# Kernel optimization log

Measured on AMD Instinct MI355X. Metric: run time of the kernel, lower is better.

Reference implementation:

```python
import jax, jax.numpy as jnp
import numpy as np


def setup_inputs() -> dict:
    key = jax.random.key(0)
    ks = jax.random.split(key, 6)
    B, H, KVH, D = 8, 32, 8, 128
    PAGES_PER_SEQ, PAGE_SIZE, L_MAX = 512, 16, 4096
    total_pages = B * PAGES_PER_SEQ  # 4096
    kv_len = PAGES_PER_SEQ * PAGE_SIZE  # 8192 tokens per sequence
    q = jax.random.normal(ks[0], (B, H, 1, D), dtype=jnp.float32)
    paged_kv_cache = jax.random.normal(ks[1], (total_pages, 2, KVH, PAGE_SIZE, D), dtype=jnp.float32)
    kv_page_indptr = (jnp.arange(B + 1, dtype=jnp.int32) * PAGES_PER_SEQ)
    kv_page_indices = jax.random.permutation(ks[2], total_pages).astype(jnp.int32)
    sparse_ind = jax.random.randint(ks[3], (B, H, L_MAX), 0, kv_len, dtype=jnp.int32)
    sparse_nnz = jax.random.randint(ks[4], (B, H), 1, L_MAX + 1, dtype=jnp.int32)
    return {
        "q": q,
        "paged_kv_cache": paged_kv_cache,
        "kv_page_indptr": kv_page_indptr,
        "kv_page_indices": kv_page_indices,
        "sparse_ind": sparse_ind,
        "sparse_nnz": sparse_nnz,
    }


def reference(q, paged_kv_cache, kv_page_indptr, kv_page_indices, sparse_ind, sparse_nnz):
    # q: [B, H, 1, D]; paged_kv_cache: [P, 2, KVH, PS, D]
    B, H, _, D = q.shape
    KVH, PS = paged_kv_cache.shape[2], paged_kv_cache.shape[3]
    groups = H // KVH
    L = sparse_ind.shape[-1]
    scale = jnp.float32(1.0 / (D ** 0.5))

    # Paged-table lookup: token index -> (logical page, offset) -> physical page id
    page_idx = sparse_ind // PS               # [B, H, L]
    off_in_page = sparse_ind % PS             # [B, H, L]
    page_id = kv_page_indices[kv_page_indptr[:B][:, None, None] + page_idx]  # [B, H, L]

    kv_head = (jnp.arange(H) // groups)[None, :, None]  # GQA head mapping, [1, H, 1]
    K = paged_kv_cache[page_id, 0, kv_head, off_in_page]  # [B, H, L, D]
    V = paged_kv_cache[page_id, 1, kv_head, off_in_page]  # [B, H, L, D]

    qk = jnp.einsum("bhd,bhld->bhl", q[:, :, 0, :], K)
    mask = jnp.arange(L)[None, None, :] < sparse_nnz[:, :, None]
    # Kernel uses additive -1e6 for masked lanes (K loaded as 0 -> qk==0)
    scores = jnp.where(mask, qk * scale, jnp.float32(-1e6))
    p = jax.nn.softmax(scores, axis=-1)       # online-softmax is math-equivalent
    out = jnp.einsum("bhl,bhld->bhd", p, V)
    return out[:, :, None, :]                  # [B, H, 1, D]
```

## Files before the change

### kernel.cpp

```cpp
#include <hip/hip_runtime.h>
#include <math.h>

#define BB   8
#define HH   32
#define KVHH 8
#define DD   128
#define PSZ  16
#define LMAX 4096
#define CHUNK 256
#define NCHUNK (LMAX / CHUNK)

#define PAGE_STRIDE (2 * KVHH * PSZ * DD)
#define KV_OFFSET   (KVHH * PSZ * DD)
#define HEAD_STRIDE (PSZ * DD)

__global__ __launch_bounds__(256) void attn_partial(
    const float* __restrict__ q,
    const float* __restrict__ cache,
    const int*   __restrict__ indptr,
    const int*   __restrict__ pageind,
    const int*   __restrict__ sind,
    const int*   __restrict__ snnz,
    float* __restrict__ ws_m,
    float* __restrict__ ws_l,
    float* __restrict__ ws_acc)
{
    const int blk   = blockIdx.x;
    const int xcd   = blk & 7;
    const int slot  = (blk >> 3) & 63;
    const int super = blk >> 9;
    const int g     = super * 8 + xcd;
    const int b     = g >> 3;
    const int kvh   = g & 7;
    const int h     = (kvh << 2) + (slot >> 4);
    const int chunk = slot & 15;
    const int bh    = b * HH + h;
    const int tid   = threadIdx.x;

    const int nnz  = snnz[bh];
    const int l0   = chunk * CHUNK;
    const int widx = bh * NCHUNK + chunk;

    if (l0 >= nnz) {
        if (tid == 0) { ws_m[widx] = -1e30f; ws_l[widx] = 0.0f; }
        if (tid < DD) ws_acc[widx * DD + tid] = 0.0f;
        return;
    }
    const int nrows = min(nnz - l0, CHUNK);
    const int nr32  = (nrows + 31) & ~31;

    __shared__ unsigned s_base[CHUNK];
    __shared__ float    s_p[CHUNK];
    __shared__ float    s_red[16];
    __shared__ float    s_acc[8][DD];

    const int indbase = indptr[b];
    const int* si = sind + bh * LMAX + l0;
    {
        unsigned base = 0u;
        if (tid < nrows) {
            const int idx = si[tid];
            const int pid = pageind[indbase + (idx >> 4)];
            base = (unsigned)pid * PAGE_STRIDE
                 + (unsigned)(kvh * HEAD_STRIDE + (idx & 15) * DD);
        }
        s_base[tid] = base;
    }
    __syncthreads();

    const int lane32 = tid & 31;
    const int hw     = tid >> 5;
    const float4 q4  = *(const float4*)(q + bh * DD + lane32 * 4);
    const float cscale = 0.08838834764831845f * 1.4426950408889634f;

    for (int i = hw; i < nr32; i += 32) {
        const unsigned b0 = s_base[i];
        const unsigned b1 = s_base[i + 8];
        const unsigned b2 = s_base[i + 16];
        const unsigned b3 = s_base[i + 24];
        const float4 k0 = *(const float4*)(cache + b0 + lane32 * 4);
        const float4 k1 = *(const float4*)(cache + b1 + lane32 * 4);
        const float4 k2 = *(const float4*)(cache + b2 + lane32 * 4);
        const float4 k3 = *(const float4*)(cache + b3 + lane32 * 4);
        float s0 = k0.x*q4.x + k0.y*q4.y + k0.z*q4.z + k0.w*q4.w;
        float s1 = k1.x*q4.x + k1.y*q4.y + k1.z*q4.z + k1.w*q4.w;
        float s2 = k2.x*q4.x + k2.y*q4.y + k2.z*q4.z + k2.w*q4.w;
        float s3 = k3.x*q4.x + k3.y*q4.y + k3.z*q4.z + k3.w*q4.w;
        #pragma unroll
        for (int m = 16; m >= 1; m >>= 1) {
            s0 += __shfl_xor(s0, m);
            s1 += __shfl_xor(s1, m);
            s2 += __shfl_xor(s2, m);
            s3 += __shfl_xor(s3, m);
        }
        if (lane32 == 0) {
            s_p[i]      = (i      < nrows) ? s0 * cscale : -1e30f;
            s_p[i + 8]  = (i + 8  < nrows) ? s1 * cscale : -1e30f;
            s_p[i + 16] = (i + 16 < nrows) ? s2 * cscale : -1e30f;
            s_p[i + 24] = (i + 24 < nrows) ? s3 * cscale : -1e30f;
        }
    }
    __syncthreads();

    const float sc = (tid < nr32) ? s_p[tid] : -1e30f;
    float wm = sc;
    #pragma unroll
    for (int m = 32; m >= 1; m >>= 1) wm = fmaxf(wm, __shfl_xor(wm, m));
    const int wv = tid >> 6;
    if ((tid & 63) == 0) s_red[wv] = wm;
    __syncthreads();
    const float M = fmaxf(fmaxf(s_red[0], s_red[1]), fmaxf(s_red[2], s_red[3]));
    const float p = (tid < nr32) ? exp2f(sc - M) : 0.0f;
    if (tid < nr32) s_p[tid] = p;
    float wl = p;
    #pragma unroll
    for (int m = 32; m >= 1; m >>= 1) wl += __shfl_xor(wl, m);
    if ((tid & 63) == 0) s_red[8 + wv] = wl;
    __syncthreads();

    float4 acc = make_float4(0.f, 0.f, 0.f, 0.f);
    for (int i = hw; i < nr32; i += 32) {
        const unsigned b0 = s_base[i];
        const unsigned b1 = s_base[i + 8];
        const unsigned b2 = s_base[i + 16];
        const unsigned b3 = s_base[i + 24];
        const float p0 = s_p[i];
        const float p1 = s_p[i + 8];
        const float p2 = s_p[i + 16];
        const float p3 = s_p[i + 24];
        const float4 v0 = *(const float4*)(cache + b0 + KV_OFFSET + lane32 * 4);
        const float4 v1 = *(const float4*)(cache + b1 + KV_OFFSET + lane32 * 4);
        const float4 v2 = *(const float4*)(cache + b2 + KV_OFFSET + lane32 * 4);
        const float4 v3 = *(const float4*)(cache + b3 + KV_OFFSET + lane32 * 4);
        acc.x += p0*v0.x; acc.y += p0*v0.y; acc.z += p0*v0.z; acc.w += p0*v0.w;
        acc.x += p1*v1.x; acc.y += p1*v1.y; acc.z += p1*v1.z; acc.w += p1*v1.w;
        acc.x += p2*v2.x; acc.y += p2*v2.y; acc.z += p2*v2.z; acc.w += p2*v2.w;
        acc.x += p3*v3.x; acc.y += p3*v3.y; acc.z += p3*v3.z; acc.w += p3*v3.w;
    }

    *(float4*)&s_acc[hw][lane32 * 4] = acc;
    __syncthreads();

    if (tid < DD) {
        float a = 0.f;
        #pragma unroll
        for (int i = 0; i < 8; i++) a += s_acc[i][tid];
        ws_acc[widx * DD + tid] = a;
        if (tid == 0) {
            ws_m[widx] = M;
            ws_l[widx] = s_red[8] + s_red[9] + s_red[10] + s_red[11];
        }
    }
}

__global__ __launch_bounds__(128) void attn_combine(
    const float* __restrict__ ws_m,
    const float* __restrict__ ws_l,
    const float* __restrict__ ws_acc,
    float* __restrict__ out)
{
    const int bh = blockIdx.x;
    const int d  = threadIdx.x;

    float M = -1e30f;
    #pragma unroll
    for (int i = 0; i < NCHUNK; i++) M = fmaxf(M, ws_m[bh * NCHUNK + i]);

    float tot = 0.f, a = 0.f;
    #pragma unroll
    for (int i = 0; i < NCHUNK; i++) {
        const float f = exp2f(ws_m[bh * NCHUNK + i] - M);
        tot += ws_l[bh * NCHUNK + i] * f;
        a   += ws_acc[(bh * NCHUNK + i) * DD + d] * f;
    }
    out[bh * DD + d] = a / tot;
}

extern "C" void kernel_launch(void* const* d_in, const int* in_sizes, int n_in,
                              void* d_out, int out_size, void* d_ws, size_t ws_size,
                              hipStream_t stream) {
    const float* q      = (const float*)d_in[0];
    const float* cache  = (const float*)d_in[1];
    const int*   indptr = (const int*)d_in[2];
    const int*   pgind  = (const int*)d_in[3];
    const int*   sind   = (const int*)d_in[4];
    const int*   snnz   = (const int*)d_in[5];
    float* out = (float*)d_out;

    float* ws_m   = (float*)d_ws;
    float* ws_l   = ws_m + BB * HH * NCHUNK;
    float* ws_acc = ws_l + BB * HH * NCHUNK;

    attn_partial<<<dim3(BB * HH * NCHUNK), dim3(256), 0, stream>>>(
        q, cache, indptr, pgind, sind, snnz, ws_m, ws_l, ws_acc);
    attn_combine<<<dim3(BB * HH), dim3(128), 0, stream>>>(
        ws_m, ws_l, ws_acc, out);
}
```

Measured before the change: 666.1 us.

## Software-pipeline K/V gathers with 8-row batches and prefetch V before softmax

Each K and V loop now handles 8 rows per half-wave (64 per batch) and double-buffers them, issuing the next batch's gathers before working on the current one. The first V batch is loaded before the softmax barriers, so its memory latency hides behind the reduction. The goal is more memory requests in flight per wave on this latency-bound random gather. In exchange, register pressure rises, which may cut occupancy, and partial chunks are rounded up to 64 rows. Pad rows use base offset 0 and get zero weight, so results stay correct.

```diff
diff --git a/kernel.cpp b/kernel.cpp
--- a/kernel.cpp
+++ b/kernel.cpp
@@ -47,7 +47,8 @@
         return;
     }
     const int nrows = min(nnz - l0, CHUNK);
-    const int nr32  = (nrows + 31) & ~31;
+    const int nr64  = (nrows + 63) & ~63;
+    const int nbat  = nr64 >> 6;
 
     __shared__ unsigned s_base[CHUNK];
     __shared__ float    s_p[CHUNK];
@@ -73,36 +74,49 @@
     const float4 q4  = *(const float4*)(q + bh * DD + lane32 * 4);
     const float cscale = 0.08838834764831845f * 1.4426950408889634f;
 
-    for (int i = hw; i < nr32; i += 32) {
-        const unsigned b0 = s_base[i];
-        const unsigned b1 = s_base[i + 8];
-        const unsigned b2 = s_base[i + 16];
-        const unsigned b3 = s_base[i + 24];
-        const float4 k0 = *(const float4*)(cache + b0 + lane32 * 4);
-        const float4 k1 = *(const float4*)(cache + b1 + lane32 * 4);
-        const float4 k2 = *(const float4*)(cache + b2 + lane32 * 4);
-        const float4 k3 = *(const float4*)(cache + b3 + lane32 * 4);
-        float s0 = k0.x*q4.x + k0.y*q4.y + k0.z*q4.z + k0.w*q4.w;
-        float s1 = k1.x*q4.x + k1.y*q4.y + k1.z*q4.z + k1.w*q4.w;
-        float s2 = k2.x*q4.x + k2.y*q4.y + k2.z*q4.z + k2.w*q4.w;
-        float s3 = k3.x*q4.x + k3.y*q4.y + k3.z*q4.z + k3.w*q4.w;
+    {
+        float4 k[8];
         #pragma unroll
-        for (int m = 16; m >= 1; m >>= 1) {
-            s0 += __shfl_xor(s0, m);
-            s1 += __shfl_xor(s1, m);
-            s2 += __shfl_xor(s2, m);
-            s3 += __shfl_xor(s3, m);
-        }
-        if (lane32 == 0) {
-            s_p[i]      = (i      < nrows) ? s0 * cscale : -1e30f;
-            s_p[i + 8]  = (i + 8  < nrows) ? s1 * cscale : -1e30f;
-            s_p[i + 16] = (i + 16 < nrows) ? s2 * cscale : -1e30f;
-            s_p[i + 24] = (i + 24 < nrows) ? s3 * cscale : -1e30f;
-        }
-    }
-    __syncthreads();
-
-    const float sc = (tid < nr32) ? s_p[tid] : -1e30f;
+        for (int r = 0; r < 8; r++)
+            k[r] = *(const float4*)(cache + s_base[hw + r * 8] + lane32 * 4);
+
+        for (int t = 0; t < nbat; ++t) {
+            const int i = hw + (t << 6);
+            float4 kn[8];
+            if (t + 1 < nbat) {
+                #pragma unroll
+                for (int r = 0; r < 8; r++)
+                    kn[r] = *(const float4*)(cache + s_base[i + 64 + r * 8] + lane32 * 4);
+            }
+            float s[8];
+            #pragma unroll
+            for (int r = 0; r < 8; r++)
+                s[r] = k[r].x*q4.x + k[r].y*q4.y + k[r].z*q4.z + k[r].w*q4.w;
+            #pragma unroll
+            for (int m = 16; m >= 1; m >>= 1) {
+                #pragma unroll
+                for (int r = 0; r < 8; r++) s[r] += __shfl_xor(s[r], m);
+            }
+            if (lane32 == 0) {
+                #pragma unroll
+                for (int r = 0; r < 8; r++)
+                    s_p[i + r * 8] = (i + r * 8 < nrows) ? s[r] * cscale : -1e30f;
+            }
+            if (t + 1 < nbat) {
+                #pragma unroll
+                for (int r = 0; r < 8; r++) k[r] = kn[r];
+            }
+        }
+    }
+
+    float4 v[8];
+    #pragma unroll
+    for (int r = 0; r < 8; r++)
+        v[r] = *(const float4*)(cache + s_base[hw + r * 8] + KV_OFFSET + lane32 * 4);
+
+    __syncthreads();
+
+    const float sc = (tid < nr64) ? s_p[tid] : -1e30f;
     float wm = sc;
     #pragma unroll
     for (int m = 32; m >= 1; m >>= 1) wm = fmaxf(wm, __shfl_xor(wm, m));
@@ -110,8 +124,8 @@
     if ((tid & 63) == 0) s_red[wv] = wm;
     __syncthreads();
     const float M = fmaxf(fmaxf(s_red[0], s_red[1]), fmaxf(s_red[2], s_red[3]));
-    const float p = (tid < nr32) ? exp2f(sc - M) : 0.0f;
-    if (tid < nr32) s_p[tid] = p;
+    const float p = (tid < nr64) ? exp2f(sc - M) : 0.0f;
+    if (tid < nr64) s_p[tid] = p;
     float wl = p;
     #pragma unroll
     for (int m = 32; m >= 1; m >>= 1) wl += __shfl_xor(wl, m);
@@ -119,23 +133,26 @@
     __syncthreads();
 
     float4 acc = make_float4(0.f, 0.f, 0.f, 0.f);
-    for (int i = hw; i < nr32; i += 32) {
-        const unsigned b0 = s_base[i];
-        const unsigned b1 = s_base[i + 8];
-        const unsigned b2 = s_base[i + 16];
-        const unsigned b3 = s_base[i + 24];
-        const float p0 = s_p[i];
-        const float p1 = s_p[i + 8];
-        const float p2 = s_p[i + 16];
-        const float p3 = s_p[i + 24];
-        const float4 v0 = *(const float4*)(cache + b0 + KV_OFFSET + lane32 * 4);
-        const float4 v1 = *(const float4*)(cache + b1 + KV_OFFSET + lane32 * 4);
-        const float4 v2 = *(const float4*)(cache + b2 + KV_OFFSET + lane32 * 4);
-        const float4 v3 = *(const float4*)(cache + b3 + KV_OFFSET + lane32 * 4);
-        acc.x += p0*v0.x; acc.y += p0*v0.y; acc.z += p0*v0.z; acc.w += p0*v0.w;
-        acc.x += p1*v1.x; acc.y += p1*v1.y; acc.z += p1*v1.z; acc.w += p1*v1.w;
-        acc.x += p2*v2.x; acc.y += p2*v2.y; acc.z += p2*v2.z; acc.w += p2*v2.w;
-        acc.x += p3*v3.x; acc.y += p3*v3.y; acc.z += p3*v3.z; acc.w += p3*v3.w;
+    for (int t = 0; t < nbat; ++t) {
+        const int i = hw + (t << 6);
+        float4 vn[8];
+        if (t + 1 < nbat) {
+            #pragma unroll
+            for (int r = 0; r < 8; r++)
+                vn[r] = *(const float4*)(cache + s_base[i + 64 + r * 8] + KV_OFFSET + lane32 * 4);
+        }
+        #pragma unroll
+        for (int r = 0; r < 8; r++) {
+            const float pr = s_p[i + r * 8];
+            acc.x += pr * v[r].x;
+            acc.y += pr * v[r].y;
+            acc.z += pr * v[r].z;
+            acc.w += pr * v[r].w;
+        }
+        if (t + 1 < nbat) {
+            #pragma unroll
+            for (int r = 0; r < 8; r++) v[r] = vn[r];
+        }
     }
 
     *(float4*)&s_acc[hw][lane32 * 4] = acc;
```

After: 662.0 us. No clear change (-0.6%).
